# Kernel tuning notes

Measured on AMD Instinct MI355X. Metric: run time of the kernel, lower is better.

The kernel has to match this reference:

```python
import jax, jax.numpy as jnp
import numpy as np

N_NODES = 100000
N_EDGES = 1200000
D = 64


def gcn_conv(x, src, dst, ew, W, b, n):
    # add self-loops with weight 1 (PyG GCNConv default)
    loops = jnp.arange(n)
    s = jnp.concatenate([src, loops])
    d = jnp.concatenate([dst, loops])
    w = jnp.concatenate([ew, jnp.ones((n,), ew.dtype)])
    deg = jax.ops.segment_sum(w, d, num_segments=n)           # [n]
    dis = jnp.where(deg > 0, jax.lax.rsqrt(deg), 0.0)
    norm = dis[s] * w * dis[d]                                # [E+n]
    h = x @ W                                                 # [n, out]
    msg = norm[:, None] * h[s]                                # gather
    out = jax.ops.segment_sum(msg, d, num_segments=n)         # scatter
    return out + b


def setup_inputs() -> dict:
    key = jax.random.key(0)
    ks = jax.random.split(key, 7)
    x = jax.random.normal(ks[0], (N_NODES, D), dtype=jnp.float32)
    edge_index = jax.random.randint(ks[1], (2, N_EDGES), 0, N_NODES, dtype=jnp.int64)
    edge_weight = jax.random.uniform(ks[2], (N_EDGES,), dtype=jnp.float32)
    W1 = jax.random.normal(ks[3], (D, D), dtype=jnp.float32) * (1.0 / np.sqrt(D))
    b1 = jnp.zeros((D,), dtype=jnp.float32)
    W2 = jax.random.normal(ks[4], (D, D), dtype=jnp.float32) * (1.0 / np.sqrt(D))
    b2 = jnp.zeros((D,), dtype=jnp.float32)
    return {"x": x, "edge_index": edge_index, "edge_weight": edge_weight,
            "W1": W1, "b1": b1, "W2": W2, "b2": b2}


def reference(x, edge_index, edge_weight, W1, b1, W2, b2):
    n = x.shape[0]
    src, dst = edge_index[0], edge_index[1]
    x1 = jax.nn.relu(gcn_conv(x, src, dst, edge_weight, W1, b1, n))
    x2 = jax.nn.relu(gcn_conv(x1, src, dst, edge_weight, W2, b2, n))
    return (x1 + x2) * 0.5
```

## Files before the change

kernel.cpp:

```cpp
#include <hip/hip_runtime.h>

#define NN 100000
#define NE 1200000
#define DD 64
#define NBUCK 196
#define BCAP 7168
#define TILE 4096
#define NB1 293
#define NB_G 1563
#define FIX25 33554432.0f
#define FIX25_INV (1.0f/33554432.0f)

typedef short bf16x8 __attribute__((ext_vector_type(8)));
typedef float f32x4  __attribute__((ext_vector_type(4)));

static __device__ __forceinline__ unsigned short f2bf(float f) {
    unsigned int u = __float_as_uint(f);
    unsigned int r = (u + 0x7fffu + ((u >> 16) & 1u)) >> 16;
    return (unsigned short)r;
}
static __device__ __forceinline__ float bf2f(unsigned short s) {
    return __uint_as_float(((unsigned int)s) << 16);
}


__global__ __launch_bounds__(256) void prep(
    int* __restrict__ cursor,
    const float* __restrict__ W1, const float* __restrict__ W2,
    unsigned short* __restrict__ Wt1, unsigned short* __restrict__ Wt2)
{
    if (blockIdx.x == 0) {
        if (threadIdx.x < NBUCK) cursor[threadIdx.x] = 0;
        return;
    }
    const float* W = (blockIdx.x == 1) ? W1 : W2;
    unsigned short* Wt = (blockIdx.x == 1) ? Wt1 : Wt2;
    int t = threadIdx.x;
    int col = t >> 2, k0 = (t & 3) * 16;
    #pragma unroll
    for (int i = 0; i < 16; ++i)
        Wt[col * 64 + k0 + i] = f2bf(W[(k0 + i) * 64 + col]);
}


static __device__ __forceinline__ void gemm_body(
    const float* __restrict__ x, const unsigned short* __restrict__ Wt,
    unsigned short* __restrict__ h16, int r0, int t,
    unsigned short* Xs, unsigned short* Ws)
{
    {
        int col = t >> 2, seg = (t & 3) * 16;
        const uint4* p = (const uint4*)(Wt + col * 64 + seg);
        uint4 a0 = p[0], a1 = p[1];
        *(uint4*)&Ws[col * 72 + seg]     = a0;
        *(uint4*)&Ws[col * 72 + seg + 8] = a1;
    }
    {
        int row = t >> 2, seg = (t & 3) * 16;
        int gr = r0 + row;
        float4 v0 = {0,0,0,0}, v1 = v0, v2 = v0, v3 = v0;
        if (gr < NN) {
            const float4* p = (const float4*)(x + (size_t)gr * DD + seg);
            v0 = p[0]; v1 = p[1]; v2 = p[2]; v3 = p[3];
        }
        ushort4 h0 = { f2bf(v0.x), f2bf(v0.y), f2bf(v0.z), f2bf(v0.w) };
        ushort4 h1 = { f2bf(v1.x), f2bf(v1.y), f2bf(v1.z), f2bf(v1.w) };
        ushort4 h2 = { f2bf(v2.x), f2bf(v2.y), f2bf(v2.z), f2bf(v2.w) };
        ushort4 h3 = { f2bf(v3.x), f2bf(v3.y), f2bf(v3.z), f2bf(v3.w) };
        *(ushort4*)&Xs[row * 72 + seg]      = h0;
        *(ushort4*)&Xs[row * 72 + seg + 4]  = h1;
        *(ushort4*)&Xs[row * 72 + seg + 8]  = h2;
        *(ushort4*)&Xs[row * 72 + seg + 12] = h3;
    }
    __syncthreads();

    const int wv = t >> 6;
    const int ln = t & 63;
    const int m  = ln & 15;
    const int q  = ln >> 4;
    const int arow = wv * 16 + m;

    bf16x8 a0 = *(const bf16x8*)&Xs[arow * 72 + q * 8];
    bf16x8 a1 = *(const bf16x8*)&Xs[arow * 72 + 32 + q * 8];

    f32x4 acc[4];
    #pragma unroll
    for (int c = 0; c < 4; ++c) {
        bf16x8 b0 = *(const bf16x8*)&Ws[(c * 16 + m) * 72 + q * 8];
        bf16x8 b1 = *(const bf16x8*)&Ws[(c * 16 + m) * 72 + 32 + q * 8];
        f32x4 z = {0.f, 0.f, 0.f, 0.f};
        z = __builtin_amdgcn_mfma_f32_16x16x32_bf16(a0, b0, z, 0, 0, 0);
        z = __builtin_amdgcn_mfma_f32_16x16x32_bf16(a1, b1, z, 0, 0, 0);
        acc[c] = z;
    }

    #pragma unroll
    for (int r = 0; r < 4; ++r) {
        int grow = r0 + wv * 16 + q * 4 + r;
        if (grow < NN) {
            #pragma unroll
            for (int c = 0; c < 4; ++c)
                h16[(size_t)grow * DD + c * 16 + m] = f2bf(acc[c][r]);
        }
    }
}


__global__ __launch_bounds__(256) void pass1_gemm(
    const int* __restrict__ src, const int* __restrict__ dst,
    const float* __restrict__ ew, int* __restrict__ cursor,
    unsigned long long* __restrict__ stage,
    const float* __restrict__ x, const unsigned short* __restrict__ Wt1,
    unsigned short* __restrict__ h16)
{
    __shared__ unsigned short Xs[64 * 72];
    __shared__ unsigned short Ws[64 * 72];
    __shared__ int cnt[NBUCK];
    __shared__ int resv[NBUCK];

    const int t = threadIdx.x;

    if (blockIdx.x >= NB1) {
        gemm_body(x, Wt1, h16, (blockIdx.x - NB1) * 64, t, Xs, Ws);
        return;
    }

    const int base = blockIdx.x * TILE;
    if (t < NBUCK) cnt[t] = 0;
    __syncthreads();

    #pragma unroll
    for (int k = 0; k < TILE / 256; ++k) {
        int e = base + k * 256 + t;
        if (e < NE) atomicAdd(&cnt[dst[e] >> 9], 1);
    }
    __syncthreads();
    if (t < NBUCK) {
        int c = cnt[t];
        resv[t] = c ? atomicAdd(&cursor[t], c) : 0;
        cnt[t] = 0;
    }
    __syncthreads();
    #pragma unroll
    for (int k = 0; k < TILE / 256; ++k) {
        int e = base + k * 256 + t;
        if (e < NE) {
            int d = dst[e];
            int b = d >> 9;
            int r = atomicAdd(&cnt[b], 1);
            int pos = resv[b] + r;
            if (pos < BCAP) {
                unsigned int meta = ((unsigned int)(d & 511) << 17) |
                                    (unsigned int)src[e];
                stage[(size_t)b * BCAP + pos] =
                    ((unsigned long long)meta << 32) | __float_as_uint(ew[e]);
            }
        }
    }
}


__global__ __launch_bounds__(512) void pass2(
    const unsigned long long* __restrict__ stage, const int* __restrict__ cursor,
    unsigned int* __restrict__ slots, unsigned int* __restrict__ degdis)
{
    __shared__ int cnt[512];
    __shared__ unsigned sum[512];

    const int b = blockIdx.x;
    const int t = threadIdx.x;
    const int n0 = b << 9;
    const int cntb = min(cursor[b], BCAP);

    cnt[t] = 0; sum[t] = 0;
    __syncthreads();

    for (int k = t; k < cntb; k += 512) {
        unsigned long long E = stage[(size_t)b * BCAP + k];
        unsigned int meta = (unsigned int)(E >> 32);
        int dl = meta >> 17;
        float w = __uint_as_float((unsigned int)E);
        int r = atomicAdd(&cnt[dl], 1);
        atomicAdd(&sum[dl], (unsigned)(w * FIX25));
        if (r < 63)
            slots[(size_t)(n0 + dl) * 64 + r] =
                ((meta & 0x1ffffu) << 15) | (f2bf(w) & 0x7fffu);
    }
    __syncthreads();

    int node = n0 + t;
    if (node < NN) {
        float deg = 1.0f + (float)sum[t] * FIX25_INV;
        float di = rsqrtf(deg);
        degdis[node] = (__float_as_uint(di) & ~63u) |
                       (unsigned)min(cnt[t], 63);
    }
}


__global__ __launch_bounds__(256) void bake(
    unsigned int* __restrict__ slots, const unsigned int* __restrict__ degdis)
{
    int i = blockIdx.x * 256 + threadIdx.x;
    int n = i >> 6, j = i & 63;
    if (n >= NN) return;
    if (j < (int)(degdis[n] & 63u)) {
        unsigned int e = slots[i];
        float dsrc = __uint_as_float(degdis[e >> 15] & ~63u);
        float nm = dsrc * bf2f((unsigned short)(e & 0x7fffu));
        slots[i] = (e & 0xffff8000u) | (f2bf(nm) & 0x7fffu);
    }
}


template <bool FINAL>
__global__ __launch_bounds__(256) void gather(
    const unsigned short* __restrict__ h16, const float* __restrict__ bias,
    const unsigned int* __restrict__ degdis, const unsigned int* __restrict__ slots,
    const float* __restrict__ prev, float* __restrict__ out)
{
    const int node = __builtin_amdgcn_readfirstlane(
        (blockIdx.x * blockDim.x + threadIdx.x) >> 6);
    const int lane = threadIdx.x & 63;
    if (node >= NN) return;

    const int g = lane >> 4;
    const int l = lane & 15;
    const int l4 = l << 2;

    const unsigned int* seg = slots + (size_t)node * 64;

    const unsigned int dd = degdis[node];
    const int deg = dd & 63;
    const float di = __uint_as_float(dd & ~63u);

    const ushort4 hs = *(const ushort4*)(h16 + (size_t)node * DD + l4);
    const float4  bb = *(const float4*)(bias + l4);
    float4 p = {0.f, 0.f, 0.f, 0.f};
    if (FINAL) p = *(const float4*)(prev + (size_t)node * DD + l4);

    f32x4 acc0 = {0,0,0,0}, acc1 = {0,0,0,0}, acc2 = {0,0,0,0}, acc3 = {0,0,0,0};

#define QUADX(q, joff, rq, nq)                                                 \
    {                                                                          \
        unsigned w0 = seg[(joff) + 4*q + 0], w1 = seg[(joff) + 4*q + 1];       \
        unsigned w2 = seg[(joff) + 4*q + 2], w3 = seg[(joff) + 4*q + 3];       \
        unsigned ea = (g & 1) ? w1 : w0;                                       \
        unsigned eb = (g & 1) ? w3 : w2;                                       \
        unsigned e  = (g & 2) ? eb : ea;                                       \
        unsigned srow = e >> 15;                                               \
        srow = (srow < NN) ? srow : 0u;                                        \
        rq = *(const ushort4*)(h16 + ((size_t)srow << 6) + l4);                \
        float nv_ = bf2f((unsigned short)(e & 0x7fffu)) * di;                  \
        nq = ((joff) + 4*q + g < deg) ? nv_ : 0.f;                             \
    }
#define FMA4(rq, nq, ac)                                                       \
    ac[0] = fmaf(nq, bf2f(rq.x), ac[0]);                                       \
    ac[1] = fmaf(nq, bf2f(rq.y), ac[1]);                                       \
    ac[2] = fmaf(nq, bf2f(rq.z), ac[2]);                                       \
    ac[3] = fmaf(nq, bf2f(rq.w), ac[3]);

    {
        ushort4 r0, r1, r2, r3;
        float n0, n1, n2, n3;
        QUADX(0, 0, r0, n0)
        QUADX(1, 0, r1, n1)
        QUADX(2, 0, r2, n2)
        QUADX(3, 0, r3, n3)
        FMA4(r0, n0, acc0)
        FMA4(r1, n1, acc1)
        FMA4(r2, n2, acc2)
        FMA4(r3, n3, acc3)
    }
    if (deg > 16) {
        for (int j = 16; j < deg; j += 16) {
            ushort4 r0, r1, r2, r3;
            float n0, n1, n2, n3;
            QUADX(0, j, r0, n0)
            QUADX(1, j, r1, n1)
            QUADX(2, j, r2, n2)
            QUADX(3, j, r3, n3)
            FMA4(r0, n0, acc0)
            FMA4(r1, n1, acc1)
            FMA4(r2, n2, acc2)
            FMA4(r3, n3, acc3)
        }
    }
#undef QUADX
#undef FMA4

    float s0 = (acc0[0] + acc1[0]) + (acc2[0] + acc3[0]);
    float s1 = (acc0[1] + acc1[1]) + (acc2[1] + acc3[1]);
    float s2 = (acc0[2] + acc1[2]) + (acc2[2] + acc3[2]);
    float s3 = (acc0[3] + acc1[3]) + (acc2[3] + acc3[3]);

    s0 += __shfl_xor(s0, 16); s1 += __shfl_xor(s1, 16);
    s2 += __shfl_xor(s2, 16); s3 += __shfl_xor(s3, 16);
    s0 += __shfl_xor(s0, 32); s1 += __shfl_xor(s1, 32);
    s2 += __shfl_xor(s2, 32); s3 += __shfl_xor(s3, 32);

    if (g == 0) {
        const float dsq = di * di;
        float v0 = fmaxf(fmaf(dsq, bf2f(hs.x), bb.x) + s0, 0.f);
        float v1 = fmaxf(fmaf(dsq, bf2f(hs.y), bb.y) + s1, 0.f);
        float v2 = fmaxf(fmaf(dsq, bf2f(hs.z), bb.z) + s2, 0.f);
        float v3 = fmaxf(fmaf(dsq, bf2f(hs.w), bb.w) + s3, 0.f);
        float4 o;
        if (FINAL) {
            o.x = 0.5f * (p.x + v0); o.y = 0.5f * (p.y + v1);
            o.z = 0.5f * (p.z + v2); o.w = 0.5f * (p.w + v3);
        } else {
            o.x = v0; o.y = v1; o.z = v2; o.w = v3;
        }
        *(float4*)(out + (size_t)node * DD + l4) = o;
    }
}

__global__ __launch_bounds__(256) void gemm_mfma(
    const float* __restrict__ x, const unsigned short* __restrict__ Wt,
    unsigned short* __restrict__ h16)
{
    __shared__ unsigned short Xs[64 * 72];
    __shared__ unsigned short Ws[64 * 72];
    gemm_body(x, Wt, h16, blockIdx.x * 64, threadIdx.x, Xs, Ws);
}


extern "C" void kernel_launch(void* const* d_in, const int* in_sizes, int n_in,
                              void* d_out, int out_size, void* d_ws, size_t ws_size,
                              hipStream_t stream) {
    const float* x   = (const float*)d_in[0];
    const int*   ei  = (const int*)d_in[1];
    const float* ewt = (const float*)d_in[2];
    const float* W1  = (const float*)d_in[3];
    const float* b1  = (const float*)d_in[4];
    const float* W2  = (const float*)d_in[5];
    const float* b2  = (const float*)d_in[6];
    float* out = (float*)d_out;

    const int* srcv = ei;
    const int* dstv = ei + NE;

    float* wsf = (float*)d_ws;
    int* cursor = (int*)wsf;
    unsigned short* Wt1 = (unsigned short*)(wsf + 256);
    unsigned short* Wt2 = Wt1 + 4096;
    unsigned int* degdis = (unsigned int*)(wsf + 4352);
    unsigned long long* stage = (unsigned long long*)(wsf + 104448);
    unsigned int* slots = (unsigned int*)(wsf + 104448 + 2 * NBUCK * BCAP);
    unsigned short* h16 = (unsigned short*)(slots + (size_t)NN * 64);

    const int GB = (NN * 64) / 256;

    prep<<<3, 256, 0, stream>>>(cursor, W1, W2, Wt1, Wt2);
    pass1_gemm<<<NB1 + NB_G, 256, 0, stream>>>(srcv, dstv, ewt, cursor, stage,
                                               x, Wt1, h16);
    pass2<<<NBUCK, 512, 0, stream>>>(stage, cursor, slots, degdis);
    bake<<<(NN * 64) / 256, 256, 0, stream>>>(slots, degdis);

    gather<false><<<GB, 256, 0, stream>>>(h16, b1, degdis, slots, nullptr, out);
    gemm_mfma<<<NB_G, 256, 0, stream>>>(out, Wt2, h16);
    gather<true><<<GB, 256, 0, stream>>>(h16, b2, degdis, slots, out, out);
}
```

Baseline: 206.3 us.

## Split h into 16-feature slabs and pin each slab to one XCD in gather

The GEMM now writes h as four column slabs of 16 bf16 features each, instead of full 64-wide rows. The gather kernel is remapped so that blockIdx&7 selects the slab. With round-robin block-to-XCD dispatch, each XCD then gathers from only one 3.2MB slab, which should fit in its L2. Each wave now handles one node for one slab, with 16 edges in parallel and 4 lanes per edge. The cost is reading each node's slot list four times, running four times as many waves with less work each, and relying on the hardware's block-to-XCD assignment for the locality gain.

```diff
diff --git a/kernel.cpp b/kernel.cpp
--- a/kernel.cpp
+++ b/kernel.cpp
@@ -45,7 +45,7 @@
 
 static __device__ __forceinline__ void gemm_body(
     const float* __restrict__ x, const unsigned short* __restrict__ Wt,
-    unsigned short* __restrict__ h16, int r0, int t,
+    unsigned short* __restrict__ hs, int r0, int t,
     unsigned short* Xs, unsigned short* Ws)
 {
     {
@@ -100,7 +100,7 @@
         if (grow < NN) {
             #pragma unroll
             for (int c = 0; c < 4; ++c)
-                h16[(size_t)grow * DD + c * 16 + m] = f2bf(acc[c][r]);
+                hs[((size_t)c * NN + grow) * 16 + m] = f2bf(acc[c][r]);
         }
     }
 }
@@ -111,7 +111,7 @@
     const float* __restrict__ ew, int* __restrict__ cursor,
     unsigned long long* __restrict__ stage,
     const float* __restrict__ x, const unsigned short* __restrict__ Wt1,
-    unsigned short* __restrict__ h16)
+    unsigned short* __restrict__ hs)
 {
     __shared__ unsigned short Xs[64 * 72];
     __shared__ unsigned short Ws[64 * 72];
@@ -121,7 +121,7 @@
     const int t = threadIdx.x;
 
     if (blockIdx.x >= NB1) {
-        gemm_body(x, Wt1, h16, (blockIdx.x - NB1) * 64, t, Xs, Ws);
+        gemm_body(x, Wt1, hs, (blockIdx.x - NB1) * 64, t, Xs, Ws);
         return;
     }
 
@@ -214,97 +214,63 @@
 
 
 template <bool FINAL>
-__global__ __launch_bounds__(256) void gather(
-    const unsigned short* __restrict__ h16, const float* __restrict__ bias,
+__global__ __launch_bounds__(512) void gather(
+    const unsigned short* __restrict__ hs, const float* __restrict__ bias,
     const unsigned int* __restrict__ degdis, const unsigned int* __restrict__ slots,
     const float* __restrict__ prev, float* __restrict__ out)
 {
+    const int bid = blockIdx.x;
+    const int xg  = bid & 7;
+    const int s   = xg & 3;
+    const int wv  = threadIdx.x >> 6;
     const int node = __builtin_amdgcn_readfirstlane(
-        (blockIdx.x * blockDim.x + threadIdx.x) >> 6);
+        (bid >> 3) * 16 + (xg >> 2) * 8 + wv);
+    if (node >= NN) return;
+
     const int lane = threadIdx.x & 63;
-    if (node >= NN) return;
-
-    const int g = lane >> 4;
-    const int l = lane & 15;
-    const int l4 = l << 2;
+    const int g  = lane >> 2;
+    const int l4 = (lane & 3) << 2;
 
     const unsigned int* seg = slots + (size_t)node * 64;
-
     const unsigned int dd = degdis[node];
     const int deg = dd & 63;
     const float di = __uint_as_float(dd & ~63u);
 
-    const ushort4 hs = *(const ushort4*)(h16 + (size_t)node * DD + l4);
-    const float4  bb = *(const float4*)(bias + l4);
+    const unsigned short* hb = hs + (size_t)s * (NN * 16);
+
+    const ushort4 hself = *(const ushort4*)(hb + (size_t)node * 16 + l4);
+    const float4  bb = *(const float4*)(bias + s * 16 + l4);
     float4 p = {0.f, 0.f, 0.f, 0.f};
-    if (FINAL) p = *(const float4*)(prev + (size_t)node * DD + l4);
-
-    f32x4 acc0 = {0,0,0,0}, acc1 = {0,0,0,0}, acc2 = {0,0,0,0}, acc3 = {0,0,0,0};
-
-#define QUADX(q, joff, rq, nq)                                                 \
-    {                                                                          \
-        unsigned w0 = seg[(joff) + 4*q + 0], w1 = seg[(joff) + 4*q + 1];       \
-        unsigned w2 = seg[(joff) + 4*q + 2], w3 = seg[(joff) + 4*q + 3];       \
-        unsigned ea = (g & 1) ? w1 : w0;                                       \
-        unsigned eb = (g & 1) ? w3 : w2;                                       \
-        unsigned e  = (g & 2) ? eb : ea;                                       \
-        unsigned srow = e >> 15;                                               \
-        srow = (srow < NN) ? srow : 0u;                                        \
-        rq = *(const ushort4*)(h16 + ((size_t)srow << 6) + l4);                \
-        float nv_ = bf2f((unsigned short)(e & 0x7fffu)) * di;                  \
-        nq = ((joff) + 4*q + g < deg) ? nv_ : 0.f;                             \
-    }
-#define FMA4(rq, nq, ac)                                                       \
-    ac[0] = fmaf(nq, bf2f(rq.x), ac[0]);                                       \
-    ac[1] = fmaf(nq, bf2f(rq.y), ac[1]);                                       \
-    ac[2] = fmaf(nq, bf2f(rq.z), ac[2]);                                       \
-    ac[3] = fmaf(nq, bf2f(rq.w), ac[3]);
-
-    {
-        ushort4 r0, r1, r2, r3;
-        float n0, n1, n2, n3;
-        QUADX(0, 0, r0, n0)
-        QUADX(1, 0, r1, n1)
-        QUADX(2, 0, r2, n2)
-        QUADX(3, 0, r3, n3)
-        FMA4(r0, n0, acc0)
-        FMA4(r1, n1, acc1)
-        FMA4(r2, n2, acc2)
-        FMA4(r3, n3, acc3)
-    }
-    if (deg > 16) {
-        for (int j = 16; j < deg; j += 16) {
-            ushort4 r0, r1, r2, r3;
-            float n0, n1, n2, n3;
-            QUADX(0, j, r0, n0)
-            QUADX(1, j, r1, n1)
-            QUADX(2, j, r2, n2)
-            QUADX(3, j, r3, n3)
-            FMA4(r0, n0, acc0)
-            FMA4(r1, n1, acc1)
-            FMA4(r2, n2, acc2)
-            FMA4(r3, n3, acc3)
-        }
-    }
-#undef QUADX
-#undef FMA4
-
-    float s0 = (acc0[0] + acc1[0]) + (acc2[0] + acc3[0]);
-    float s1 = (acc0[1] + acc1[1]) + (acc2[1] + acc3[1]);
-    float s2 = (acc0[2] + acc1[2]) + (acc2[2] + acc3[2]);
-    float s3 = (acc0[3] + acc1[3]) + (acc2[3] + acc3[3]);
-
-    s0 += __shfl_xor(s0, 16); s1 += __shfl_xor(s1, 16);
-    s2 += __shfl_xor(s2, 16); s3 += __shfl_xor(s3, 16);
-    s0 += __shfl_xor(s0, 32); s1 += __shfl_xor(s1, 32);
-    s2 += __shfl_xor(s2, 32); s3 += __shfl_xor(s3, 32);
+    if (FINAL) p = *(const float4*)(prev + (size_t)node * DD + s * 16 + l4);
+
+    f32x4 acc = {0.f, 0.f, 0.f, 0.f};
+    for (int j = 0; j < deg; j += 16) {
+        unsigned int e = seg[j + g];
+        unsigned int srow = e >> 15;
+        srow = (srow < NN) ? srow : 0u;
+        ushort4 hv = *(const ushort4*)(hb + (size_t)srow * 16 + l4);
+        float nv = bf2f((unsigned short)(e & 0x7fffu)) * di;
+        nv = (j + g < deg) ? nv : 0.f;
+        acc[0] = fmaf(nv, bf2f(hv.x), acc[0]);
+        acc[1] = fmaf(nv, bf2f(hv.y), acc[1]);
+        acc[2] = fmaf(nv, bf2f(hv.z), acc[2]);
+        acc[3] = fmaf(nv, bf2f(hv.w), acc[3]);
+    }
+
+    #pragma unroll
+    for (int off = 4; off <= 32; off <<= 1) {
+        acc[0] += __shfl_xor(acc[0], off);
+        acc[1] += __shfl_xor(acc[1], off);
+        acc[2] += __shfl_xor(acc[2], off);
+        acc[3] += __shfl_xor(acc[3], off);
+    }
 
     if (g == 0) {
         const float dsq = di * di;
-        float v0 = fmaxf(fmaf(dsq, bf2f(hs.x), bb.x) + s0, 0.f);
-        float v1 = fmaxf(fmaf(dsq, bf2f(hs.y), bb.y) + s1, 0.f);
-        float v2 = fmaxf(fmaf(dsq, bf2f(hs.z), bb.z) + s2, 0.f);
-        float v3 = fmaxf(fmaf(dsq, bf2f(hs.w), bb.w) + s3, 0.f);
+        float v0 = fmaxf(fmaf(dsq, bf2f(hself.x), bb.x) + acc[0], 0.f);
+        float v1 = fmaxf(fmaf(dsq, bf2f(hself.y), bb.y) + acc[1], 0.f);
+        float v2 = fmaxf(fmaf(dsq, bf2f(hself.z), bb.z) + acc[2], 0.f);
+        float v3 = fmaxf(fmaf(dsq, bf2f(hself.w), bb.w) + acc[3], 0.f);
         float4 o;
         if (FINAL) {
             o.x = 0.5f * (p.x + v0); o.y = 0.5f * (p.y + v1);
@@ -312,17 +278,17 @@
         } else {
             o.x = v0; o.y = v1; o.z = v2; o.w = v3;
         }
-        *(float4*)(out + (size_t)node * DD + l4) = o;
+        *(float4*)(out + (size_t)node * DD + s * 16 + l4) = o;
     }
 }
 
 __global__ __launch_bounds__(256) void gemm_mfma(
     const float* __restrict__ x, const unsigned short* __restrict__ Wt,
-    unsigned short* __restrict__ h16)
+    unsigned short* __restrict__ hs)
 {
     __shared__ unsigned short Xs[64 * 72];
     __shared__ unsigned short Ws[64 * 72];
-    gemm_body(x, Wt, h16, blockIdx.x * 64, threadIdx.x, Xs, Ws);
+    gemm_body(x, Wt, hs, blockIdx.x * 64, threadIdx.x, Xs, Ws);
 }
 
 
@@ -348,17 +314,17 @@
     unsigned int* degdis = (unsigned int*)(wsf + 4352);
     unsigned long long* stage = (unsigned long long*)(wsf + 104448);
     unsigned int* slots = (unsigned int*)(wsf + 104448 + 2 * NBUCK * BCAP);
-    unsigned short* h16 = (unsigned short*)(slots + (size_t)NN * 64);
-
-    const int GB = (NN * 64) / 256;
+    unsigned short* hs = (unsigned short*)(slots + (size_t)NN * 64);
+
+    const int GB = 6250 * 8;
 
     prep<<<3, 256, 0, stream>>>(cursor, W1, W2, Wt1, Wt2);
     pass1_gemm<<<NB1 + NB_G, 256, 0, stream>>>(srcv, dstv, ewt, cursor, stage,
-                                               x, Wt1, h16);
+                                               x, Wt1, hs);
     pass2<<<NBUCK, 512, 0, stream>>>(stage, cursor, slots, degdis);
     bake<<<(NN * 64) / 256, 256, 0, stream>>>(slots, degdis);
 
-    gather<false><<<GB, 256, 0, stream>>>(h16, b1, degdis, slots, nullptr, out);
-    gemm_mfma<<<NB_G, 256, 0, stream>>>(out, Wt2, h16);
-    gather<true><<<GB, 256, 0, stream>>>(h16, b2, degdis, slots, out, out);
-}
+    gather<false><<<GB, 512, 0, stream>>>(hs, b1, degdis, slots, nullptr, out);
+    gemm_mfma<<<NB_G, 256, 0, stream>>>(out, Wt2, hs);
+    gather<true><<<GB, 512, 0, stream>>>(hs, b2, degdis, slots, out, out);
+}
```

After: 356.2 us. +72.7%, slower.
